# Performance work log

Measured on AMD Instinct MI355X. Metric: run time of the kernel, lower is better.

Reference implementation:

```python
import jax, jax.numpy as jnp
import numpy as np


def setup_inputs() -> dict:
    key = jax.random.key(0)
    k1, k2, k3, k4 = jax.random.split(key, 4)
    B, Q, K, H, D = 2, 2048, 2048, 16, 128
    qs = jax.random.normal(k1, (B, Q, H, D), dtype=jnp.float32)
    ks = jax.random.normal(k2, (B, K, H, D), dtype=jnp.float32)
    vs = jax.random.normal(k3, (B, K, H, D), dtype=jnp.float32)
    valid_lens = jax.random.randint(k4, (B,), 1, K + 1, dtype=jnp.int32)
    return {"qs": qs, "ks": ks, "vs": vs, "valid_lens": valid_lens}


def reference(qs, ks, vs, valid_lens):
    B, Q, H, D = qs.shape
    K = ks.shape[1]
    # rearrange 'B L H D -> (B H) L D'
    q = qs.transpose(0, 2, 1, 3).reshape(B * H, Q, D)
    k = ks.transpose(0, 2, 1, 3).reshape(B * H, K, D)
    v = vs.transpose(0, 2, 1, 3).reshape(B * H, K, D)
    # DotScorer: scaled dot product -> (B*H, Q, K)
    scores = jnp.einsum('bqd,bkd->bqk', q, k) / jnp.sqrt(jnp.float32(D))
    # mask_attn: key positions >= valid_len get large negative score
    vl = jnp.repeat(valid_lens, H)                         # (B*H,)
    mask = jnp.arange(K)[None, None, :] < vl[:, None, None]
    scores = jnp.where(mask, scores, jnp.float32(-1e6))
    attn = jax.nn.softmax(scores, axis=-1)
    # dropout is identity (p_dropout=0 / not training)
    ctx = attn @ v                                         # (B*H, Q, D)
    ctx = ctx.reshape(B, H, Q, D).transpose(0, 2, 1, 3)    # (B, Q, H, D)
    return ctx, attn.reshape(B, H, Q, K)
```

## Files before the change

kernel.cpp:

```cpp
#include <hip/hip_runtime.h>
#include <hip/hip_bf16.h>
#include <stdint.h>

#define B_ 2
#define Qn 2048
#define Kn 2048
#define Hn 16
#define Dn 128
#define QT 128
#define HD (Hn*Dn)

typedef __bf16 bf16x8 __attribute__((ext_vector_type(8)));
typedef __bf16 bf16x4 __attribute__((ext_vector_type(4)));
typedef float f32x4 __attribute__((ext_vector_type(4)));
typedef float f32x16 __attribute__((ext_vector_type(16)));
typedef unsigned short u16x8 __attribute__((ext_vector_type(8)));

union BF8 { __bf16 e[8]; bf16x8 v; };
union U16x8 { unsigned short u[8]; u16x8 v; };

#define SCALE 0.088388347648318447f
#define SCL2  (0.088388347648318447f * 1.4426950408889634f)

#if __has_builtin(__builtin_amdgcn_exp2f)
#define EXP2(x) __builtin_amdgcn_exp2f(x)
#else
#define EXP2(x) exp2f(x)
#endif

__device__ __forceinline__ bf16x4 cvt4(f32x4 a) {
  bf16x4 r;
  r[0] = (__bf16)a[0]; r[1] = (__bf16)a[1];
  r[2] = (__bf16)a[2]; r[3] = (__bf16)a[3];
  return r;
}

__global__ __launch_bounds__(256) void conv_kv(const float* __restrict__ ks,
                                               const float* __restrict__ vs,
                                               const int* __restrict__ vlen,
                                               unsigned short* __restrict__ kws,
                                               unsigned short* __restrict__ vws) {
  __shared__ unsigned short l[64 * 132];
  const int tid = threadIdx.x;
  if (blockIdx.x < 512) {
    const int blk = blockIdx.x;
    const int bh = blk >> 4, t = blk & 15;
    const int b = bh >> 4, h = bh & 15;
    const int nkt = (vlen[b] + 63) >> 6;
    if (t * 2 >= nkt) return;
    const float* src = ks + ((size_t)(b * Kn + t * 128) * Hn + h) * Dn;
    unsigned short* dst = kws + (size_t)blk * 16384;
    #pragma unroll
    for (int i = 0; i < 8; ++i) {
      int idx = i * 256 + tid;
      int row = idx >> 4, sp = idx & 15;
      int slot = (sp - row) & 15;
      const float* s2 = src + (size_t)row * HD + slot * 8;
      f32x4 a0 = *(const f32x4*)s2;
      f32x4 a1 = *(const f32x4*)(s2 + 4);
      U16x8 o;
      *(bf16x4*)&o.u[0] = cvt4(a0);
      *(bf16x4*)&o.u[4] = cvt4(a1);
      *(u16x8*)(dst + (size_t)idx * 8) = o.v;
    }
  } else {
    const int blk = blockIdx.x - 512;
    const int bh = blk >> 5, t = blk & 31;
    const int b = bh >> 4, h = bh & 15;
    const int nkt = (vlen[b] + 63) >> 6;
    if (t >= nkt) return;
    const float* src = vs + ((size_t)(b * Kn + t * 64) * Hn + h) * Dn;
    #pragma unroll
    for (int i = 0; i < 8; ++i) {
      int idx = i * 256 + tid;
      int k = idx >> 5, dc = idx & 31;
      f32x4 a = *(const f32x4*)(src + (size_t)k * HD + dc * 4);
      *(bf16x4*)&l[k * 132 + dc * 4] = cvt4(a);
    }
    __syncthreads();
    unsigned short* dst = vws + (size_t)blk * 8192;
    #pragma unroll
    for (int i = 0; i < 4; ++i) {
      int idx = i * 256 + tid;
      int d = idx >> 3, ds = idx & 7;
      int c = (ds - d) & 7;
      int kb = ((c >> 2) * 32) + (((c >> 1) & 1) * 16) + ((c & 1) * 4);
      U16x8 o;
      #pragma unroll
      for (int j = 0; j < 4; ++j) {
        o.u[j]     = l[(kb + j) * 132 + d];
        o.u[4 + j] = l[(kb + 8 + j) * 132 + d];
      }
      *(u16x8*)(dst + (size_t)idx * 8) = o.v;
    }
  }
}

__device__ __forceinline__ void dma16(const void* g, void* l) {
  __builtin_amdgcn_global_load_lds((const __attribute__((address_space(1))) void*)g,
                                   (__attribute__((address_space(3))) void*)l, 16, 0, 0);
}
__device__ __forceinline__ void dma_tile(const char* gsrc, char* lds, int tid, int n4k) {
  const int off  = tid * 16;
  const int woff = (tid & 192) * 16;
  #pragma unroll
  for (int i = 0; i < n4k; ++i)
    dma16(gsrc + i * 4096 + off, lds + i * 4096 + woff);
}

#define WAIT0BAR do { \
  asm volatile("s_waitcnt vmcnt(0)" ::: "memory"); \
  __builtin_amdgcn_s_barrier(); \
  __builtin_amdgcn_sched_barrier(0); } while (0)

#define WAIT16BAR do { \
  asm volatile("s_waitcnt vmcnt(16)" ::: "memory"); \
  __builtin_amdgcn_s_barrier(); \
  __builtin_amdgcn_sched_barrier(0); } while (0)

__global__ __launch_bounds__(256, 2) void attn_fwd(
    const float* __restrict__ qs, const int* __restrict__ vlen,
    const char* __restrict__ kimg, const char* __restrict__ vimg,
    float* __restrict__ ctx_out, float* __restrict__ attn_out)
{
  __shared__ __align__(16) char smraw[65536];

  const int tid = threadIdx.x, wave = tid >> 6, lane = tid & 63;
  const int l31 = lane & 31, hi = lane >> 5;

  const int L   = blockIdx.x;
  const int xcd = L & 7;
  const int i5  = L >> 3;
  const int bh  = ((i5 & 3) << 3) + xcd;
  const int qt  = i5 >> 2;
  const int b   = bh >> 4, h = bh & 15;
  const int vl  = vlen[b];
  const int qbw = qt * QT + wave * 32;

  int vaddrK[8], vaddrV[4];
  #pragma unroll
  for (int s = 0; s < 8; ++s)
    vaddrK[s] = l31 * 256 + (((2 * s + hi + l31) & 15) << 4);
  #pragma unroll
  for (int jj = 0; jj < 4; ++jj)
    vaddrV[jj] = l31 * 128 + ((((hi + 2 * jj) + l31) & 7) << 4);

  BF8 qf[8];
  {
    const float* qrow = qs + (((size_t)(b * Qn + qbw + l31)) * Hn + h) * Dn;
    #pragma unroll
    for (int s = 0; s < 8; ++s) {
      int d0 = s * 16 + hi * 8;
      f32x4 a0 = *(const f32x4*)(qrow + d0);
      f32x4 a1 = *(const f32x4*)(qrow + d0 + 4);
      #pragma unroll
      for (int jj = 0; jj < 4; ++jj) {
        qf[s].e[jj]     = (__bf16)(a0[jj] * SCL2);
        qf[s].e[4 + jj] = (__bf16)(a1[jj] * SCL2);
      }
    }
  }

  const char* kimg_bh = kimg + ((size_t)(bh * 16) << 15);
  const char* vimg_bh = vimg + ((size_t)(bh * 32) << 14);

  const int nkt  = (vl + 63) >> 6;
  const int nkt2 = (vl + 127) >> 7;
  const int col0 = nkt * 64;

  f32x4 rsv = {0.f, 0.f, 0.f, 0.f};
  f32x16 ctxa[4];
  #pragma unroll
  for (int ch = 0; ch < 4; ++ch)
    #pragma unroll
    for (int i = 0; i < 16; ++i) ctxa[ch][i] = 0.f;

  {
    const bool hasb = (vl & 63) != 0;
    dma_tile(kimg_bh, smraw, tid, 4);
    dma_tile(vimg_bh, smraw + 32768, tid, 4);
    WAIT0BAR;
    for (int t = 0; t < nkt; ++t) {
      const int cur = t & 1;
      if (t + 1 < nkt) {
        const int tn = t + 1;
        dma_tile(kimg_bh + ((size_t)(tn >> 1) << 15) + ((size_t)(tn & 1) << 14),
                 smraw + ((cur ^ 1) << 14), tid, 4);
        dma_tile(vimg_bh + ((size_t)tn << 14), smraw + 32768 + ((cur ^ 1) << 14), tid, 4);
      }
      const bool mb = hasb && (t == nkt - 1);
      const char* kb_l = smraw + (cur << 14);
      const char* vb_l = smraw + 32768 + (cur << 14);
      #pragma unroll
      for (int m = 0; m < 2; ++m) {
        f32x16 acc;
        #pragma unroll
        for (int i = 0; i < 16; ++i) acc[i] = 0.f;
        #pragma unroll
        for (int s = 0; s < 8; ++s) {
          BF8 kf; kf.v = *(const bf16x8*)(kb_l + m * 8192 + vaddrK[s]);
          acc = __builtin_amdgcn_mfma_f32_32x32x16_bf16(kf.v, qf[s].v, acc, 0, 0, 0);
        }
        const int kb0 = t * 64 + m * 32;
        BF8 pf0, pf1;
        #pragma unroll
        for (int r4 = 0; r4 < 4; ++r4) {
          #pragma unroll
          for (int rr = 0; rr < 4; ++rr) {
            float e;
            if (!mb) e = EXP2(acc[r4 * 4 + rr]);
            else {
              int key = kb0 + r4 * 8 + hi * 4 + rr;
              e = (key < vl) ? EXP2(acc[r4 * 4 + rr]) : 0.f;
            }
            rsv[rr] += e;
            if (r4 < 2) pf0.e[r4 * 4 + rr] = (__bf16)e;
            else        pf1.e[(r4 - 2) * 4 + rr] = (__bf16)e;
          }
        }
        #pragma unroll
        for (int ch = 0; ch < 4; ++ch) {
          BF8 v0; v0.v = *(const bf16x8*)(vb_l + ch * 4096 + vaddrV[2 * m]);
          ctxa[ch] = __builtin_amdgcn_mfma_f32_32x32x16_bf16(v0.v, pf0.v, ctxa[ch], 0, 0, 0);
          BF8 v1; v1.v = *(const bf16x8*)(vb_l + ch * 4096 + vaddrV[2 * m + 1]);
          ctxa[ch] = __builtin_amdgcn_mfma_f32_32x32x16_bf16(v1.v, pf1.v, ctxa[ch], 0, 0, 0);
        }
      }
      WAIT0BAR;
    }
  }
  float rs = (rsv[0] + rsv[1]) + (rsv[2] + rsv[3]);
  rs += __shfl_xor(rs, 32);
  const float inv = 1.0f / rs;

  {
    const f32x4 z4 = {0.f, 0.f, 0.f, 0.f};
    #pragma unroll 1
    for (int r = 0; r < 32; ++r) {
      float* zp = attn_out + ((size_t)bh * Qn + qbw + r) * Kn;
      for (int c4 = col0 + lane * 4; c4 < Kn; c4 += 256)
        *(f32x4*)(zp + c4) = z4;
    }
  }

  {
    const bool hasb2 = (vl & 127) != 0;
    dma_tile(kimg_bh, smraw, tid, 8);
    WAIT0BAR;
    float* rowp = attn_out + ((size_t)bh * Qn + qbw + l31) * Kn;
    for (int t = 0; t < nkt2; ++t) {
      const int cur = t & 1;
      if (t + 1 < nkt2)
        dma_tile(kimg_bh + ((size_t)(t + 1) << 15), smraw + ((cur ^ 1) << 15), tid, 8);
      const bool mb = hasb2 && (t == nkt2 - 1);
      const char* kb_l = smraw + (cur << 15);
      #pragma unroll
      for (int m = 0; m < 4; ++m) {
        f32x16 acc;
        #pragma unroll
        for (int i = 0; i < 16; ++i) acc[i] = 0.f;
        #pragma unroll
        for (int s = 0; s < 8; ++s) {
          BF8 kf; kf.v = *(const bf16x8*)(kb_l + m * 8192 + vaddrK[s]);
          acc = __builtin_amdgcn_mfma_f32_32x32x16_bf16(kf.v, qf[s].v, acc, 0, 0, 0);
        }
        const int kb0 = t * 128 + m * 32;
        #pragma unroll
        for (int r4 = 0; r4 < 4; ++r4) {
          f32x4 p;
          if (!mb) {
            #pragma unroll
            for (int rr = 0; rr < 4; ++rr) p[rr] = EXP2(acc[r4 * 4 + rr]) * inv;
          } else {
            #pragma unroll
            for (int rr = 0; rr < 4; ++rr) {
              int key = kb0 + r4 * 8 + hi * 4 + rr;
              p[rr] = (key < vl) ? EXP2(acc[r4 * 4 + rr]) * inv : 0.f;
            }
          }
          *(f32x4*)(rowp + kb0 + r4 * 8 + hi * 4) = p;
        }
      }
      WAIT16BAR;
    }
  }

  float* cp = ctx_out + (((size_t)(b * Qn + qbw + l31)) * Hn + h) * Dn;
  #pragma unroll
  for (int ch = 0; ch < 4; ++ch)
    #pragma unroll
    for (int r4 = 0; r4 < 4; ++r4) {
      f32x4 o;
      #pragma unroll
      for (int rr = 0; rr < 4; ++rr) o[rr] = ctxa[ch][r4 * 4 + rr] * inv;
      *(f32x4*)(cp + ch * 32 + r4 * 8 + hi * 4) = o;
    }
}

#define KT 64
#define KT1 128
#define KROW 132
#define VROW 72
struct SMp2f { unsigned short K[2][KT][KROW]; unsigned short V[2][Dn][VROW]; };
union SMuf { SMp2f p2; unsigned short K1[2][KT1][KROW]; };

__device__ __forceinline__ void bar_lgkm() {
  asm volatile("s_waitcnt lgkmcnt(0)" ::: "memory");
  __builtin_amdgcn_s_barrier();
  __builtin_amdgcn_sched_barrier(0);
}
__device__ __forceinline__ void fb_stage_k64(const float* kb, unsigned short (*dst)[KROW], int tid) {
  #pragma unroll
  for (int ii = 0; ii < 8; ++ii) {
    int chunk = ii * 256 + tid;
    int row = chunk >> 5, cv = chunk & 31;
    f32x4 a = *(const f32x4*)(kb + (size_t)row * HD + cv * 4);
    *(bf16x4*)&dst[row][cv * 4] = cvt4(a);
  }
}
__device__ __forceinline__ void fb_stage_k128(const float* kb, unsigned short (*dst)[KROW], int tid) {
  #pragma unroll
  for (int ii = 0; ii < 16; ++ii) {
    int chunk = ii * 256 + tid;
    int row = chunk >> 5, cv = chunk & 31;
    f32x4 a = *(const f32x4*)(kb + (size_t)row * HD + cv * 4);
    *(bf16x4*)&dst[row][cv * 4] = cvt4(a);
  }
}
__device__ __forceinline__ void fb_stage_v64(const float* vb, unsigned short (*dst)[VROW], int tid) {
  int d = tid & 127, t0 = tid >> 7;
  const float* colp = vb + d;
  #pragma unroll
  for (int rr = 0; rr < 4; ++rr) {
    int idx = rr * 2 + t0;
    int base = (idx >> 2) * 32 + ((idx >> 1) & 1) * 16 + (idx & 1) * 4;
    BF8 t;
    #pragma unroll
    for (int jj = 0; jj < 4; ++jj) {
      t.e[jj]     = (__bf16)colp[(size_t)(base + jj) * HD];
      t.e[4 + jj] = (__bf16)colp[(size_t)(base + 8 + jj) * HD];
    }
    *(bf16x8*)&dst[d][idx * 8] = t.v;
  }
}
__global__ __launch_bounds__(256, 2) void attn_fwd_fb(
    const float* __restrict__ qs, const float* __restrict__ ks,
    const float* __restrict__ vs, const int* __restrict__ vlen,
    float* __restrict__ ctx_out, float* __restrict__ attn_out)
{
  __shared__ __align__(16) SMuf sm;
  const int tid = threadIdx.x, wave = tid >> 6, lane = tid & 63;
  const int l31 = lane & 31, hi = lane >> 5;
  const int L = blockIdx.x, xcd = L & 7, i5 = L >> 3;
  const int bh = ((i5 & 3) << 3) + xcd, qt = i5 >> 2;
  const int b = bh >> 4, h = bh & 15;
  const int vl = vlen[b];
  const int qbw = qt * QT + wave * 32;
  BF8 qf[8];
  {
    const float* qrow = qs + (((size_t)(b * Qn + qbw + l31)) * Hn + h) * Dn;
    #pragma unroll
    for (int s = 0; s < 8; ++s) {
      int d0 = s * 16 + hi * 8;
      f32x4 a0 = *(const f32x4*)(qrow + d0);
      f32x4 a1 = *(const f32x4*)(qrow + d0 + 4);
      #pragma unroll
      for (int jj = 0; jj < 4; ++jj) {
        qf[s].e[jj] = (__bf16)(a0[jj] * SCL2);
        qf[s].e[4 + jj] = (__bf16)(a1[jj] * SCL2);
      }
    }
  }
  const float* kbase = ks + ((size_t)b * Kn * Hn + h) * Dn;
  const float* vbase = vs + ((size_t)b * Kn * Hn + h) * Dn;
  f32x4 rsv = {0.f, 0.f, 0.f, 0.f};
  {
    const int nkt1 = (vl + KT1 - 1) / KT1;
    const bool hasb1 = (vl & (KT1 - 1)) != 0;
    fb_stage_k128(kbase, sm.K1[0], tid);
    bar_lgkm();
    for (int t = 0; t < nkt1; ++t) {
      const int cur = t & 1;
      if (t + 1 < nkt1) fb_stage_k128(kbase + (size_t)(t + 1) * KT1 * HD, sm.K1[cur ^ 1], tid);
      const bool mb = hasb1 && (t == nkt1 - 1);
      #pragma unroll
      for (int m = 0; m < 4; ++m) {
        f32x16 acc;
        #pragma unroll
        for (int i = 0; i < 16; ++i) acc[i] = 0.f;
        #pragma unroll
        for (int s = 0; s < 8; ++s) {
          BF8 kf; kf.v = *(const bf16x8*)&sm.K1[cur][m * 32 + l31][s * 16 + hi * 8];
          acc = __builtin_amdgcn_mfma_f32_32x32x16_bf16(kf.v, qf[s].v, acc, 0, 0, 0);
        }
        if (!mb) {
          #pragma unroll
          for (int reg = 0; reg < 16; ++reg) rsv[reg & 3] += EXP2(acc[reg]);
        } else {
          const int kb0 = t * KT1 + m * 32 + hi * 4;
          #pragma unroll
          for (int reg = 0; reg < 16; ++reg) {
            int key = kb0 + (reg & 3) + 8 * (reg >> 2);
            rsv[reg & 3] += (key < vl) ? EXP2(acc[reg]) : 0.f;
          }
        }
      }
      bar_lgkm();
    }
  }
  float rs = (rsv[0] + rsv[1]) + (rsv[2] + rsv[3]);
  rs += __shfl_xor(rs, 32);
  const float inv = 1.0f / rs;
  f32x16 ctxa[4];
  #pragma unroll
  for (int ch = 0; ch < 4; ++ch)
    #pragma unroll
    for (int i = 0; i < 16; ++i) ctxa[ch][i] = 0.f;
  const int nkt = (vl + KT - 1) / KT;
  const bool hasb2 = (vl & (KT - 1)) != 0;
  fb_stage_k64(kbase, sm.p2.K[0], tid);
  fb_stage_v64(vbase, sm.p2.V[0], tid);
  bar_lgkm();
  float* rowp = attn_out + ((size_t)bh * Qn + qbw + l31) * Kn;
  for (int t = 0; t < nkt; ++t) {
    const int cur = t & 1;
    if (t + 1 < nkt) {
      fb_stage_k64(kbase + (size_t)(t + 1) * KT * HD, sm.p2.K[cur ^ 1], tid);
      fb_stage_v64(vbase + (size_t)(t + 1) * KT * HD, sm.p2.V[cur ^ 1], tid);
    }
    const bool mb = hasb2 && (t == nkt - 1);
    #pragma unroll
    for (int m = 0; m < 2; ++m) {
      f32x16 acc;
      #pragma unroll
      for (int i = 0; i < 16; ++i) acc[i] = 0.f;
      #pragma unroll
      for (int s = 0; s < 8; ++s) {
        BF8 kf; kf.v = *(const bf16x8*)&sm.p2.K[cur][m * 32 + l31][s * 16 + hi * 8];
        acc = __builtin_amdgcn_mfma_f32_32x32x16_bf16(kf.v, qf[s].v, acc, 0, 0, 0);
      }
      const int kb0 = t * KT + m * 32;
      BF8 pf0, pf1;
      #pragma unroll
      for (int r4 = 0; r4 < 4; ++r4) {
        f32x4 p;
        if (!mb) {
          #pragma unroll
          for (int rr = 0; rr < 4; ++rr) p[rr] = EXP2(acc[r4 * 4 + rr]) * inv;
        } else {
          #pragma unroll
          for (int rr = 0; rr < 4; ++rr) {
            int key = kb0 + r4 * 8 + hi * 4 + rr;
            p[rr] = (key < vl) ? EXP2(acc[r4 * 4 + rr]) * inv : 0.f;
          }
        }
        #pragma unroll
        for (int rr = 0; rr < 4; ++rr) {
          if (r4 < 2) pf0.e[r4 * 4 + rr] = (__bf16)p[rr];
          else        pf1.e[(r4 - 2) * 4 + rr] = (__bf16)p[rr];
        }
        *(f32x4*)(rowp + kb0 + r4 * 8 + hi * 4) = p;
      }
      #pragma unroll
      for (int ch = 0; ch < 4; ++ch) {
        BF8 v0; v0.v = *(const bf16x8*)&sm.p2.V[cur][ch * 32 + l31][(m * 4 + hi) * 8];
        ctxa[ch] = __builtin_amdgcn_mfma_f32_32x32x16_bf16(v0.v, pf0.v, ctxa[ch], 0, 0, 0);
        BF8 v1; v1.v = *(const bf16x8*)&sm.p2.V[cur][ch * 32 + l31][(m * 4 + 2 + hi) * 8];
        ctxa[ch] = __builtin_amdgcn_mfma_f32_32x32x16_bf16(v1.v, pf1.v, ctxa[ch], 0, 0, 0);
      }
    }
    bar_lgkm();
  }
  const int col0 = nkt * KT;
  #pragma unroll 1
  for (int r = 0; r < 32; ++r) {
    float* zp = attn_out + ((size_t)bh * Qn + qbw + r) * Kn;
    for (int c4 = col0 + lane * 4; c4 < Kn; c4 += 256)
      *(f32x4*)(zp + c4) = (f32x4){0.f, 0.f, 0.f, 0.f};
  }
  float* cp = ctx_out + (((size_t)(b * Qn + qbw + l31)) * Hn + h) * Dn;
  #pragma unroll
  for (int ch = 0; ch < 4; ++ch)
    #pragma unroll
    for (int r4 = 0; r4 < 4; ++r4) {
      f32x4 o;
      #pragma unroll
      for (int rr = 0; rr < 4; ++rr) o[rr] = ctxa[ch][r4 * 4 + rr];
      *(f32x4*)(cp + ch * 32 + r4 * 8 + hi * 4) = o;
    }
}

extern "C" void kernel_launch(void* const* d_in, const int* in_sizes, int n_in,
                              void* d_out, int out_size, void* d_ws, size_t ws_size,
                              hipStream_t stream) {
  const float* qs   = (const float*)d_in[0];
  const float* ks   = (const float*)d_in[1];
  const float* vs   = (const float*)d_in[2];
  const int*   vlen = (const int*)d_in[3];
  float* ctx  = (float*)d_out;
  float* attn = ctx + (size_t)B_ * Qn * Hn * Dn;

  if (ws_size >= ((size_t)32 << 20)) {
    unsigned short* kws = (unsigned short*)d_ws;
    unsigned short* vws = kws + ((size_t)8 << 20);
    conv_kv<<<dim3(1536), 256, 0, stream>>>(ks, vs, vlen, kws, vws);
    attn_fwd<<<dim3((Qn / QT) * B_ * Hn), 256, 0, stream>>>(
        qs, vlen, (const char*)kws, (const char*)vws, ctx, attn);
  } else {
    attn_fwd_fb<<<dim3((Qn / QT) * B_ * Hn), 256, 0, stream>>>(qs, ks, vs, vlen, ctx, attn);
  }
}
```

Baseline: 186.0 us.

## Shrink LDS tiles to 48KB to fit three blocks per CU

The shared-memory footprint drops from 64KB to 48KB and launch bounds go to 3 blocks per CU, so more workgroups can be resident. To make that fit, pass 1 now streams K in 32-key tiles while V stays in 64-key tiles reloaded every other step, and pass 2 uses 64-key K tiles with a matching vmcnt wait. The aim is more latency hiding through occupancy, paid for with more loop iterations, more barriers per key, and tighter register pressure under the new bound.

```diff
diff --git a/kernel.cpp b/kernel.cpp
--- a/kernel.cpp
+++ b/kernel.cpp
@@ -113,17 +113,17 @@
   __builtin_amdgcn_s_barrier(); \
   __builtin_amdgcn_sched_barrier(0); } while (0)
 
-#define WAIT16BAR do { \
-  asm volatile("s_waitcnt vmcnt(16)" ::: "memory"); \
+#define WAIT8BAR do { \
+  asm volatile("s_waitcnt vmcnt(8)" ::: "memory"); \
   __builtin_amdgcn_s_barrier(); \
   __builtin_amdgcn_sched_barrier(0); } while (0)
 
-__global__ __launch_bounds__(256, 2) void attn_fwd(
+__global__ __launch_bounds__(256, 3) void attn_fwd(
     const float* __restrict__ qs, const int* __restrict__ vlen,
     const char* __restrict__ kimg, const char* __restrict__ vimg,
     float* __restrict__ ctx_out, float* __restrict__ attn_out)
 {
-  __shared__ __align__(16) char smraw[65536];
+  __shared__ __align__(16) char smraw[49152];
 
   const int tid = threadIdx.x, wave = tid >> 6, lane = tid & 63;
   const int l31 = lane & 31, hi = lane >> 5;
@@ -164,9 +164,9 @@
   const char* kimg_bh = kimg + ((size_t)(bh * 16) << 15);
   const char* vimg_bh = vimg + ((size_t)(bh * 32) << 14);
 
-  const int nkt  = (vl + 63) >> 6;
-  const int nkt2 = (vl + 127) >> 7;
-  const int col0 = nkt * 64;
+  const int nkt32 = (vl + 31) >> 5;
+  const int nkt2  = (vl + 63) >> 6;
+  const int col0  = nkt32 * 32;
 
   f32x4 rsv = {0.f, 0.f, 0.f, 0.f};
   f32x16 ctxa[4];
@@ -176,55 +176,57 @@
     for (int i = 0; i < 16; ++i) ctxa[ch][i] = 0.f;
 
   {
-    const bool hasb = (vl & 63) != 0;
-    dma_tile(kimg_bh, smraw, tid, 4);
-    dma_tile(vimg_bh, smraw + 32768, tid, 4);
+    const bool hasb = (vl & 31) != 0;
+    dma_tile(kimg_bh, smraw, tid, 2);
+    dma_tile(vimg_bh, smraw + 16384, tid, 4);
     WAIT0BAR;
-    for (int t = 0; t < nkt; ++t) {
-      const int cur = t & 1;
-      if (t + 1 < nkt) {
+    for (int t = 0; t < nkt32; ++t) {
+      const int kcur = t & 1;
+      const int vcur = (t >> 1) & 1;
+      if (t + 1 < nkt32) {
         const int tn = t + 1;
-        dma_tile(kimg_bh + ((size_t)(tn >> 1) << 15) + ((size_t)(tn & 1) << 14),
-                 smraw + ((cur ^ 1) << 14), tid, 4);
-        dma_tile(vimg_bh + ((size_t)tn << 14), smraw + 32768 + ((cur ^ 1) << 14), tid, 4);
-      }
-      const bool mb = hasb && (t == nkt - 1);
-      const char* kb_l = smraw + (cur << 14);
-      const char* vb_l = smraw + 32768 + (cur << 14);
-      #pragma unroll
-      for (int m = 0; m < 2; ++m) {
-        f32x16 acc;
-        #pragma unroll
-        for (int i = 0; i < 16; ++i) acc[i] = 0.f;
-        #pragma unroll
-        for (int s = 0; s < 8; ++s) {
-          BF8 kf; kf.v = *(const bf16x8*)(kb_l + m * 8192 + vaddrK[s]);
-          acc = __builtin_amdgcn_mfma_f32_32x32x16_bf16(kf.v, qf[s].v, acc, 0, 0, 0);
-        }
-        const int kb0 = t * 64 + m * 32;
-        BF8 pf0, pf1;
-        #pragma unroll
-        for (int r4 = 0; r4 < 4; ++r4) {
-          #pragma unroll
-          for (int rr = 0; rr < 4; ++rr) {
-            float e;
-            if (!mb) e = EXP2(acc[r4 * 4 + rr]);
-            else {
-              int key = kb0 + r4 * 8 + hi * 4 + rr;
-              e = (key < vl) ? EXP2(acc[r4 * 4 + rr]) : 0.f;
-            }
-            rsv[rr] += e;
-            if (r4 < 2) pf0.e[r4 * 4 + rr] = (__bf16)e;
-            else        pf1.e[(r4 - 2) * 4 + rr] = (__bf16)e;
+        dma_tile(kimg_bh + ((size_t)(tn >> 2) << 15) + ((size_t)(tn & 3) << 13),
+                 smraw + ((kcur ^ 1) << 13), tid, 2);
+        if (!(tn & 1))
+          dma_tile(vimg_bh + ((size_t)(tn >> 1) << 14),
+                   smraw + 16384 + ((vcur ^ 1) << 14), tid, 4);
+      }
+      const bool mb = hasb && (t == nkt32 - 1);
+      const char* kb_l = smraw + (kcur << 13);
+      const char* vb_l = smraw + 16384 + (vcur << 14);
+      const int p = t & 1;
+
+      f32x16 acc;
+      #pragma unroll
+      for (int i = 0; i < 16; ++i) acc[i] = 0.f;
+      #pragma unroll
+      for (int s = 0; s < 8; ++s) {
+        BF8 kf; kf.v = *(const bf16x8*)(kb_l + vaddrK[s]);
+        acc = __builtin_amdgcn_mfma_f32_32x32x16_bf16(kf.v, qf[s].v, acc, 0, 0, 0);
+      }
+      const int kb0 = t * 32;
+      BF8 pf0, pf1;
+      #pragma unroll
+      for (int r4 = 0; r4 < 4; ++r4) {
+        #pragma unroll
+        for (int rr = 0; rr < 4; ++rr) {
+          float e;
+          if (!mb) e = EXP2(acc[r4 * 4 + rr]);
+          else {
+            int key = kb0 + r4 * 8 + hi * 4 + rr;
+            e = (key < vl) ? EXP2(acc[r4 * 4 + rr]) : 0.f;
           }
-        }
-        #pragma unroll
-        for (int ch = 0; ch < 4; ++ch) {
-          BF8 v0; v0.v = *(const bf16x8*)(vb_l + ch * 4096 + vaddrV[2 * m]);
-          ctxa[ch] = __builtin_amdgcn_mfma_f32_32x32x16_bf16(v0.v, pf0.v, ctxa[ch], 0, 0, 0);
-          BF8 v1; v1.v = *(const bf16x8*)(vb_l + ch * 4096 + vaddrV[2 * m + 1]);
-          ctxa[ch] = __builtin_amdgcn_mfma_f32_32x32x16_bf16(v1.v, pf1.v, ctxa[ch], 0, 0, 0);
-        }
+          rsv[rr] += e;
+          if (r4 < 2) pf0.e[r4 * 4 + rr] = (__bf16)e;
+          else        pf1.e[(r4 - 2) * 4 + rr] = (__bf16)e;
+        }
+      }
+      #pragma unroll
+      for (int ch = 0; ch < 4; ++ch) {
+        BF8 v0; v0.v = *(const bf16x8*)(vb_l + ch * 4096 + vaddrV[2 * p]);
+        ctxa[ch] = __builtin_amdgcn_mfma_f32_32x32x16_bf16(v0.v, pf0.v, ctxa[ch], 0, 0, 0);
+        BF8 v1; v1.v = *(const bf16x8*)(vb_l + ch * 4096 + vaddrV[2 * p + 1]);
+        ctxa[ch] = __builtin_amdgcn_mfma_f32_32x32x16_bf16(v1.v, pf1.v, ctxa[ch], 0, 0, 0);
       }
       WAIT0BAR;
     }
@@ -244,18 +246,21 @@
   }
 
   {
-    const bool hasb2 = (vl & 127) != 0;
-    dma_tile(kimg_bh, smraw, tid, 8);
+    const bool hasb2 = (vl & 63) != 0;
+    dma_tile(kimg_bh, smraw, tid, 4);
     WAIT0BAR;
     float* rowp = attn_out + ((size_t)bh * Qn + qbw + l31) * Kn;
     for (int t = 0; t < nkt2; ++t) {
       const int cur = t & 1;
-      if (t + 1 < nkt2)
-        dma_tile(kimg_bh + ((size_t)(t + 1) << 15), smraw + ((cur ^ 1) << 15), tid, 8);
+      if (t + 1 < nkt2) {
+        const int tn = t + 1;
+        dma_tile(kimg_bh + ((size_t)(tn >> 1) << 15) + ((size_t)(tn & 1) << 14),
+                 smraw + ((cur ^ 1) << 14), tid, 4);
+      }
       const bool mb = hasb2 && (t == nkt2 - 1);
-      const char* kb_l = smraw + (cur << 15);
-      #pragma unroll
-      for (int m = 0; m < 4; ++m) {
+      const char* kb_l = smraw + (cur << 14);
+      #pragma unroll
+      for (int m = 0; m < 2; ++m) {
         f32x16 acc;
         #pragma unroll
         for (int i = 0; i < 16; ++i) acc[i] = 0.f;
@@ -264,7 +269,7 @@
           BF8 kf; kf.v = *(const bf16x8*)(kb_l + m * 8192 + vaddrK[s]);
           acc = __builtin_amdgcn_mfma_f32_32x32x16_bf16(kf.v, qf[s].v, acc, 0, 0, 0);
         }
-        const int kb0 = t * 128 + m * 32;
+        const int kb0 = t * 64 + m * 32;
         #pragma unroll
         for (int r4 = 0; r4 < 4; ++r4) {
           f32x4 p;
@@ -281,7 +286,7 @@
           *(f32x4*)(rowp + kb0 + r4 * 8 + hi * 4) = p;
         }
       }
-      WAIT16BAR;
+      WAIT8BAR;
     }
   }
 
```

New measurement: 220.2 us. 1.18x slower.
